# Optimization experiments

Measured on AMD Instinct MI355X. Metric: run time of the kernel, lower is better.

The kernel has to match this reference:

```python
import jax, jax.numpy as jnp
import numpy as np

SEQ, BATCH, D, N = 256, 4, 512, 32768
TEMP = 0.5


def setup_inputs() -> dict:
    key = jax.random.key(0)
    ks = jax.random.split(key, 16)
    d = D
    # xavier_uniform with gain 1/sqrt(2) for square [d,d]: limit = gain*sqrt(6/(d+d))
    lim_t = (1.0 / np.sqrt(2.0)) * np.sqrt(6.0 / (d + d))
    lim_g1 = np.sqrt(6.0 / (2 * d + d))  # default kaiming-ish scale approximated by xavier
    lim_g2 = np.sqrt(6.0 / (d + 1))
    inp = {
        "q": jax.random.normal(ks[0], (SEQ, BATCH, D), dtype=jnp.float32),
        "prev_layer_output": jax.random.normal(ks[1], (SEQ, BATCH, D), dtype=jnp.float32),
        "Wq": jax.random.uniform(ks[2], (D, D), jnp.float32, -lim_t, lim_t),
        "bq": jnp.zeros((D,), jnp.float32),
        "Wk": jax.random.uniform(ks[3], (D, D), jnp.float32, -lim_t, lim_t),
        "bk": jnp.zeros((D,), jnp.float32),
        "Wv": jax.random.uniform(ks[4], (D, D), jnp.float32, -lim_t, lim_t),
        "bv": jnp.zeros((D,), jnp.float32),
        "Wg1": jax.random.uniform(ks[5], (D, 2 * D), jnp.float32, -lim_g1, lim_g1),
        "bg1": jnp.zeros((D,), jnp.float32),
        "Wg2": jax.random.uniform(ks[6], (1, D), jnp.float32, -lim_g2, lim_g2),
        "bg2": jnp.zeros((1,), jnp.float32),
        "dstore_k": jax.random.normal(ks[7], (N, D), dtype=jnp.float32),
        "dstore_v": jax.random.normal(ks[8], (N, D), dtype=jnp.float32),
    }
    return inp


def reference(q, prev_layer_output, Wq, bq, Wk, bk, Wv, bv, Wg1, bg1, Wg2, bg2, dstore_k, dstore_v):
    # [S,B,D] -> [B,S,D]
    qb = jnp.transpose(q, (1, 0, 2))
    prevb = jnp.transpose(prev_layer_output, (1, 0, 2))
    # enable_tune projections
    _q = qb @ Wq.T + bq                      # [B,S,D]
    _k = dstore_k @ Wk.T + bk                # [N,D]
    _v = dstore_v @ Wv.T + bv                # [N,D]
    _q = _q * (D ** -0.5)
    # attention over datastore, temperature-scaled softmax
    logits = jnp.einsum("bsd,nd->bsn", _q, _k) / TEMP  # [B,S,N]
    w = jax.nn.softmax(logits, axis=-1)
    attn = jnp.einsum("bsn,nd->bsd", w, _v)            # [B,S,D]
    # gated residual fusion
    cat = jnp.concatenate([attn, prevb], axis=-1)      # [B,S,2D]
    h = jax.nn.relu(cat @ Wg1.T + bg1)                 # [B,S,D]
    sigma = jax.nn.sigmoid(h @ Wg2.T + bg2)            # [B,S,1]
    res = attn * sigma + prevb * (1.0 - sigma)
    return jnp.transpose(res, (1, 0, 2))               # [S,B,D]
```

## Files before the change

### kernel.cpp

```cpp
#include <hip/hip_runtime.h>
#include <hip/hip_bf16.h>
#include <cstdint>
#include <cstddef>


typedef unsigned short u16;
typedef u16    u16x8 __attribute__((ext_vector_type(8)));
typedef u16    u16x4 __attribute__((ext_vector_type(4)));
typedef __bf16 bf16x8 __attribute__((ext_vector_type(8)));
typedef float  f32x4 __attribute__((ext_vector_type(4)));

#define MFMA16(a, b, c) __builtin_amdgcn_mfma_f32_16x16x32_bf16( \
    __builtin_bit_cast(bf16x8, (a)), __builtin_bit_cast(bf16x8, (b)), (c), 0, 0, 0)

#define AS1 __attribute__((address_space(1)))
#define AS3 __attribute__((address_space(3)))

__device__ __forceinline__ u16 f2bf(float f) {
  unsigned u = __builtin_bit_cast(unsigned, f);
  u += 0x7fffu + ((u >> 16) & 1u);
  return (u16)(u >> 16);
}

__device__ __forceinline__ void dma16(const u16* g, u16* l) {
  __builtin_amdgcn_global_load_lds((const AS1 unsigned int*)g,
                                   (AS3 unsigned int*)l, 16, 0, 0);
}

__global__ __launch_bounds__(256) void prep_all(
    const float* __restrict__ dk, const float* __restrict__ dv,
    const float* __restrict__ Wq, const float* __restrict__ Wk,
    const float* __restrict__ bk, const float* __restrict__ bq,
    u16* __restrict__ kbf, u16* __restrict__ vt, float* __restrict__ zbase,
    float* __restrict__ cqvec, float* __restrict__ b2pre,
    float* __restrict__ cq0) {
  const int bx = blockIdx.x, t = threadIdx.x;
  if (bx < 4096) {
    __shared__ u16 Lt[64 * 72];
    const int n0 = (bx & 511) * 64, d0 = (bx >> 9) * 64;
    const int n = t >> 2, c4 = t & 3;
#pragma unroll
    for (int i = 0; i < 4; i++) {
      int col = (c4 + 4 * i) * 4;
      float4 x = *(const float4*)(dv + (size_t)(n0 + n) * 512 + d0 + col);
      Lt[(col + 0) * 72 + n] = f2bf(x.x);
      Lt[(col + 1) * 72 + n] = f2bf(x.y);
      Lt[(col + 2) * 72 + n] = f2bf(x.z);
      Lt[(col + 3) * 72 + n] = f2bf(x.w);
    }
    __syncthreads();
#pragma unroll
    for (int u = 0; u < 2; u++) {
      int unit = t + 256 * u;
      int d = unit >> 3, un = unit & 7;
      *(u16x8*)(vt + (size_t)(d0 + d) * 32768 + n0 + un * 8) =
          *(const u16x8*)&Lt[d * 72 + un * 8];
    }
  } else if (bx < 8192) {
    const int j = bx - 4096;
    size_t i0 = ((size_t)j * 256 + t) * 16;
#pragma unroll
    for (int u = 0; u < 4; u++) {
      float4 v = *(const float4*)(dk + i0 + u * 4);
      u16x4 o = {f2bf(v.x), f2bf(v.y), f2bf(v.z), f2bf(v.w)};
      *(u16x4*)(kbf + i0 + u * 4) = o;
    }
    int zi = j * 256 + t;
    if (zi < 131584) ((float4*)zbase)[zi] = make_float4(0.f, 0.f, 0.f, 0.f);
  } else if (bx < 8194) {
    int e = (bx - 8192) * 256 + t;
    float s1 = 0.f, s2 = 0.f;
    for (int d = 0; d < 512; d++) {
      s1 += bk[d] * Wq[d * 512 + e];
      s2 += bq[d] * Wk[d * 512 + e];
    }
    cqvec[e] = s1;
    b2pre[e] = s2;
  } else {
    __shared__ float red[4];
    float s = 0.f;
    for (int d = t; d < 512; d += 256) s += bq[d] * bk[d];
#pragma unroll
    for (int off = 32; off; off >>= 1) s += __shfl_down(s, off, 64);
    if ((t & 63) == 0) red[t >> 6] = s;
    __syncthreads();
    if (t == 0) cq0[0] = 0.0883883476483184f * (red[0] + red[1] + red[2] + red[3]);
  }
}

template <bool TRANSA, bool TRANSB, bool CONCAT, bool RELU, bool OUTBF16,
          bool ROWSCALE, bool CQ, bool GATE, int KK>
__global__ __launch_bounds__(256, 2) void gemm64(
    const float* __restrict__ A, const float* __restrict__ A2,
    const float* __restrict__ B, const float* __restrict__ bias,
    const float* __restrict__ lvec, const float* __restrict__ bkv,
    const float* __restrict__ wg2, float alpha, void* __restrict__ Cv,
    float* __restrict__ cqout, const float* __restrict__ cq0buf,
    float* __restrict__ sdot) {
  __shared__ u16 As[64 * 72];
  __shared__ u16 Bs[64 * 72];
  const int tid = threadIdx.x;
  const int w = tid >> 6, lane = tid & 63, quad = lane >> 4, l15 = lane & 15;
  const int m0 = blockIdx.y * 64, n0 = blockIdx.x * 64;
  const int arow = tid >> 2, ac4 = tid & 3;
  float rs = 1.0f;
  if (ROWSCALE) rs = 1.0f / lvec[m0 + arow];
  const bool docq = CQ && (blockIdx.x == 0);
  float cqacc = 0.f;
  const f32x4 fzero = {0.f, 0.f, 0.f, 0.f};
  f32x4 acc[4];
#pragma unroll
  for (int i = 0; i < 4; i++) acc[i] = fzero;

  float4 ra[4], rb[4], rk[4];
  auto loadA = [&](int k0) {
    const float* src;
    if (TRANSA)
      src = A + (size_t)(k0 + arow) * 512 + m0;
    else if (CONCAT)
      src = (k0 < 512) ? (A + (size_t)(m0 + arow) * 512 + k0)
                       : (A2 + (size_t)(m0 + arow) * 512 + (k0 - 512));
    else
      src = A + (size_t)(m0 + arow) * KK + k0;
#pragma unroll
    for (int i = 0; i < 4; i++) ra[i] = *(const float4*)(src + (ac4 + 4 * i) * 4);
  };
  auto loadB = [&](int k0) {
    const float* src = TRANSB ? (B + (size_t)(n0 + arow) * KK + k0)
                              : (B + (size_t)(k0 + arow) * 512 + n0);
#pragma unroll
    for (int i = 0; i < 4; i++) rb[i] = *(const float4*)(src + (ac4 + 4 * i) * 4);
  };
  auto loadK = [&](int k0) {
#pragma unroll
    for (int i = 0; i < 4; i++) rk[i] = *(const float4*)(bkv + k0 + (ac4 + 4 * i) * 4);
  };

  loadA(0);
  loadB(0);
  if (docq) loadK(0);
#pragma unroll
  for (int k0 = 0; k0 < KK; k0 += 64) {
    __syncthreads();
#pragma unroll
    for (int i = 0; i < 4; i++) {
      int col = (ac4 + 4 * i) * 4;
      float4 x = ra[i];
      if (ROWSCALE) { x.x *= rs; x.y *= rs; x.z *= rs; x.w *= rs; }
      if (TRANSA) {
        As[(col + 0) * 72 + arow] = f2bf(x.x);
        As[(col + 1) * 72 + arow] = f2bf(x.y);
        As[(col + 2) * 72 + arow] = f2bf(x.z);
        As[(col + 3) * 72 + arow] = f2bf(x.w);
      } else {
        u16x4 oa = {f2bf(x.x), f2bf(x.y), f2bf(x.z), f2bf(x.w)};
        *(u16x4*)&As[arow * 72 + col] = oa;
      }
      float4 y = rb[i];
      if (TRANSB) {
        u16x4 ob = {f2bf(y.x), f2bf(y.y), f2bf(y.z), f2bf(y.w)};
        *(u16x4*)&Bs[arow * 72 + col] = ob;
      } else {
        Bs[(col + 0) * 72 + arow] = f2bf(y.x);
        Bs[(col + 1) * 72 + arow] = f2bf(y.y);
        Bs[(col + 2) * 72 + arow] = f2bf(y.z);
        Bs[(col + 3) * 72 + arow] = f2bf(y.w);
      }
      if (docq)
        cqacc += ra[i].x * rk[i].x + ra[i].y * rk[i].y + ra[i].z * rk[i].z +
                 ra[i].w * rk[i].w;
    }
    if (k0 + 64 < KK) {
      loadA(k0 + 64);
      loadB(k0 + 64);
      if (docq) loadK(k0 + 64);
    }
    __syncthreads();
#pragma unroll
    for (int ks = 0; ks < 2; ks++) {
      u16x8 af = *(const u16x8*)&As[(w * 16 + l15) * 72 + ks * 32 + quad * 8];
#pragma unroll
      for (int nt = 0; nt < 4; nt++) {
        u16x8 bf = *(const u16x8*)&Bs[(nt * 16 + l15) * 72 + ks * 32 + quad * 8];
        acc[nt] = MFMA16(af, bf, acc[nt]);
      }
    }
  }

  if (docq) {
    cqacc += __shfl_xor(cqacc, 1, 64);
    cqacc += __shfl_xor(cqacc, 2, 64);
    if (ac4 == 0) cqout[m0 + arow] = alpha * cqacc + cq0buf[0];
  }
  if (GATE) {
    float part[4] = {0.f, 0.f, 0.f, 0.f};
#pragma unroll
    for (int nt = 0; nt < 4; nt++) {
      int col = n0 + nt * 16 + l15;
      float b = bias[col], wv = wg2[col];
#pragma unroll
      for (int i = 0; i < 4; i++) part[i] += fmaxf((acc[nt][i] + b) * alpha, 0.f) * wv;
    }
#pragma unroll
    for (int i = 0; i < 4; i++) {
      float v = part[i];
      v += __shfl_xor(v, 1, 64); v += __shfl_xor(v, 2, 64);
      v += __shfl_xor(v, 4, 64); v += __shfl_xor(v, 8, 64);
      if (l15 == 0) atomicAdd(&sdot[m0 + w * 16 + quad * 4 + i], v);
    }
  } else {
#pragma unroll
    for (int nt = 0; nt < 4; nt++) {
      int col = n0 + nt * 16 + l15;
      float b = bias ? bias[col] : 0.f;
#pragma unroll
      for (int i = 0; i < 4; i++) {
        int row = m0 + w * 16 + quad * 4 + i;
        float y = (acc[nt][i] + b) * alpha;
        if (RELU) y = fmaxf(y, 0.f);
        if (OUTBF16)
          ((u16*)Cv)[(size_t)row * 512 + col] = f2bf(y);
        else
          ((float*)Cv)[(size_t)row * 512 + col] = y;
      }
    }
  }
}

__global__ __launch_bounds__(512, 2) void flash(
    const u16* __restrict__ kbf,
    const u16* __restrict__ vt,
    const u16* __restrict__ q2,
    const float* __restrict__ cq,
    float* __restrict__ racc,
    float* __restrict__ lacc) {
  __shared__ u16 Ks[2][64 * 520];
  __shared__ u16 Es[2][64 * 72];
  const int tid = threadIdx.x;
  const int w = tid >> 6, lane = tid & 63, quad = lane >> 4, l15 = lane & 15;
  const int bx = blockIdx.x;
  const int xcd = bx & 7, idx = bx >> 3;
  const int qt = idx & 15, half = idx >> 4;
  const int rowbase = (xcd * 2 + half) * 2048;
  const int qbase = qt * 64;
  const int qh = w & 1, nq = w >> 1;
  const int colb = w * 64;

  u16x8 qf[2][16];
  float cqs[2];
#pragma unroll
  for (int st = 0; st < 2; st++) {
    const u16* qp = q2 + (size_t)(qbase + qh * 32 + st * 16 + l15) * 512 + quad * 8;
#pragma unroll
    for (int ks = 0; ks < 16; ks++) qf[st][ks] = *(const u16x8*)(qp + ks * 32);
    cqs[st] = cq[qbase + qh * 32 + st * 16 + l15];
  }
  const f32x4 fzero = {0.f, 0.f, 0.f, 0.f};
  f32x4 acc[4][4];
#pragma unroll
  for (int a = 0; a < 4; a++)
#pragma unroll
    for (int b = 0; b < 4; b++) acc[a][b] = fzero;
  float lp[2] = {0.f, 0.f};

  auto dma_sub = [&](int sub) {
    u16* dst = &Ks[sub & 1][(w * 8) * 520];
    const u16* g = kbf + (size_t)(rowbase + sub * 64 + w * 8) * 512 + lane * 8;
#pragma unroll
    for (int j = 0; j < 8; j++) dma16(g + (size_t)j * 512, dst + j * 520);
  };

  dma_sub(0);
  __builtin_amdgcn_s_waitcnt(0);
  __syncthreads();

#pragma unroll 1
  for (int sub = 0; sub < 32; ++sub) {
    const int buf = sub & 1;
    const int n0 = rowbase + sub * 64;
    if (sub + 1 < 32) dma_sub(sub + 1);
    u16x8 bvp[2][4];
#pragma unroll
    for (int nk = 0; nk < 2; nk++)
#pragma unroll
      for (int ct = 0; ct < 4; ct++)
        bvp[nk][ct] = *(const u16x8*)(vt + (size_t)(colb + ct * 16 + l15) * 32768 +
                                      n0 + nk * 32 + quad * 8);
    f32x4 sa[2][2];
    sa[0][0] = fzero; sa[0][1] = fzero; sa[1][0] = fzero; sa[1][1] = fzero;
#pragma unroll
    for (int ks = 0; ks < 16; ks++) {
      u16x8 af = *(const u16x8*)&Ks[buf][(nq * 16 + l15) * 520 + ks * 32 + quad * 8];
      sa[0][ks & 1] = MFMA16(af, qf[0][ks], sa[0][ks & 1]);
      sa[1][ks & 1] = MFMA16(af, qf[1][ks], sa[1][ks & 1]);
    }
#pragma unroll
    for (int st = 0; st < 2; st++) {
      f32x4 sv = sa[st][0] + sa[st][1];
      u16x4 pk;
      float ls = 0.f;
#pragma unroll
      for (int i = 0; i < 4; i++) {
        float e = __expf(sv[i] + cqs[st]);
        ls += e;
        pk[i] = f2bf(e);
      }
      lp[st] += ls;
      *(u16x4*)&Es[buf][(qh * 32 + st * 16 + l15) * 72 + nq * 16 + quad * 4] = pk;
    }
    __builtin_amdgcn_s_waitcnt(0);
    __syncthreads();
#pragma unroll
    for (int nk = 0; nk < 2; nk++) {
      u16x8 ef[4];
#pragma unroll
      for (int q2i = 0; q2i < 4; q2i++)
        ef[q2i] = *(const u16x8*)&Es[buf][(q2i * 16 + l15) * 72 + nk * 32 + quad * 8];
#pragma unroll
      for (int ct = 0; ct < 4; ct++)
#pragma unroll
        for (int q2i = 0; q2i < 4; q2i++)
          acc[q2i][ct] = MFMA16(ef[q2i], bvp[nk][ct], acc[q2i][ct]);
    }
  }
#pragma unroll
  for (int q2i = 0; q2i < 4; q2i++)
#pragma unroll
    for (int ct = 0; ct < 4; ct++) {
      int col = colb + ct * 16 + l15;
#pragma unroll
      for (int i = 0; i < 4; i++) {
        int row = qbase + q2i * 16 + quad * 4 + i;
        atomicAdd(&racc[(size_t)row * 512 + col], acc[q2i][ct][i]);
      }
    }
#pragma unroll
  for (int st = 0; st < 2; st++) {
    float v = lp[st];
    v += __shfl_xor(v, 16, 64);
    v += __shfl_xor(v, 32, 64);
    if (quad == 0) atomicAdd(&lacc[qbase + qh * 32 + st * 16 + l15], v);
  }
}

__global__ __launch_bounds__(128) void finalize(
    const float* __restrict__ sdot, const float* __restrict__ bg2,
    const float* __restrict__ attn, const float* __restrict__ prev,
    float* __restrict__ out) {
  int r = blockIdx.x, t = threadIdx.x;
  float sg = 1.f / (1.f + __expf(-(sdot[r] + bg2[0])));
  float4 a = ((const float4*)(attn + (size_t)r * 512))[t];
  float4 p = ((const float4*)(prev + (size_t)r * 512))[t];
  float4 o = {a.x * sg + p.x * (1.f - sg), a.y * sg + p.y * (1.f - sg),
              a.z * sg + p.z * (1.f - sg), a.w * sg + p.w * (1.f - sg)};
  ((float4*)(out + (size_t)r * 512))[t] = o;
}

extern "C" void kernel_launch(void* const* d_in, const int* in_sizes, int n_in,
                              void* d_out, int out_size, void* d_ws, size_t ws_size,
                              hipStream_t stream) {
  const float* q    = (const float*)d_in[0];
  const float* prev = (const float*)d_in[1];
  const float* Wq   = (const float*)d_in[2];
  const float* bq   = (const float*)d_in[3];
  const float* Wk   = (const float*)d_in[4];
  const float* bk   = (const float*)d_in[5];
  const float* Wv   = (const float*)d_in[6];
  const float* bv   = (const float*)d_in[7];
  const float* Wg1  = (const float*)d_in[8];
  const float* bg1  = (const float*)d_in[9];
  const float* Wg2  = (const float*)d_in[10];
  const float* bg2  = (const float*)d_in[11];
  const float* dk   = (const float*)d_in[12];
  const float* dv   = (const float*)d_in[13];
  float* out = (float*)d_out;

  char* ws = (char*)d_ws;
  u16*   kbf   = (u16*)(ws);
  u16*   vt    = (u16*)(ws + 33554432);
  float* racc  = (float*)(ws + 67108864);
  float* lacc  = (float*)(ws + 69206016);
  float* sdot  = (float*)(ws + 69210112);
  float* cqv   = (float*)(ws + 69214208);
  u16*   q2    = (u16*)(ws + 69218304);
  float* Wqk   = (float*)(ws + 70266880);
  float* cqvec = (float*)(ws + 71315456);
  float* b2pre = (float*)(ws + 71317504);
  float* cq0   = (float*)(ws + 71319552);
  float* attn  = (float*)(ws + 72364032);

  prep_all<<<8195, 256, 0, stream>>>(dk, dv, Wq, Wk, bk, bq, kbf, vt, racc,
                                     cqvec, b2pre, cq0);
  gemm64<true, false, false, false, false, false, false, false, 512>
      <<<dim3(8, 8), 256, 0, stream>>>(Wq, nullptr, Wk, nullptr, nullptr,
                                       nullptr, nullptr, 1.0f, Wqk, nullptr,
                                       nullptr, nullptr);
  gemm64<false, false, false, false, true, false, true, false, 512>
      <<<dim3(8, 16), 256, 0, stream>>>(q, nullptr, Wqk, b2pre, nullptr, cqvec,
                                        nullptr, 0.0883883476483184f, q2, cqv,
                                        cq0, nullptr);
  flash<<<256, 512, 0, stream>>>(kbf, vt, q2, cqv, racc, lacc);
  gemm64<false, true, false, false, false, true, false, false, 512>
      <<<dim3(8, 16), 256, 0, stream>>>(racc, nullptr, Wv, bv, lacc, nullptr,
                                        nullptr, 1.0f, attn, nullptr, nullptr,
                                        nullptr);
  gemm64<false, true, true, true, false, false, false, true, 1024>
      <<<dim3(8, 16), 256, 0, stream>>>(attn, prev, Wg1, bg1, nullptr, nullptr,
                                        Wg2, 1.0f, nullptr, nullptr, nullptr,
                                        sdot);
  finalize<<<1024, 128, 0, stream>>>(sdot, bg2, attn, prev, out);
}
```

Measured before the change: 475.8 us.

## Switch datastore attention to FP8 MFMA with chunked partials and fused prep

Converts K, V and the projected queries to FP8 (e4m3) and runs both attention matmuls with FP8 MFMA. Queries are staged in swizzled LDS, while K rows are read straight from global memory. The flash kernel now splits the datastore into 32 chunks and writes bf16 partial outputs, which a new reduce kernel sums, replacing float atomics on the output. The Wq·Wk GEMM and the bias-vector work are folded into the prep launch. The per-query bias constant is dropped because softmax normalisation cancels it. The aim is to halve the bytes moved for K/V and to use the higher FP8 MFMA throughput. The cost is much lower precision in the logits and exp weights, plus an extra partial-buffer round trip.

New measurement: 492.7 us. +3.6%, slower.

```diff
diff --git a/kernel.cpp b/kernel.cpp
--- a/kernel.cpp
+++ b/kernel.cpp
@@ -1,118 +1,62 @@
 #include <hip/hip_runtime.h>
-#include <hip/hip_bf16.h>
 #include <cstdint>
 #include <cstddef>
 
 
 typedef unsigned short u16;
-typedef u16    u16x8 __attribute__((ext_vector_type(8)));
+typedef unsigned char u8;
+typedef u8     u8x8  __attribute__((ext_vector_type(8)));
+typedef u8     u8x16 __attribute__((ext_vector_type(16)));
 typedef u16    u16x4 __attribute__((ext_vector_type(4)));
 typedef __bf16 bf16x8 __attribute__((ext_vector_type(8)));
 typedef float  f32x4 __attribute__((ext_vector_type(4)));
 
 #define MFMA16(a, b, c) __builtin_amdgcn_mfma_f32_16x16x32_bf16( \
     __builtin_bit_cast(bf16x8, (a)), __builtin_bit_cast(bf16x8, (b)), (c), 0, 0, 0)
-
-#define AS1 __attribute__((address_space(1)))
-#define AS3 __attribute__((address_space(3)))
+#define MFMA8(a, b, c) \
+    __builtin_amdgcn_mfma_f32_16x16x32_fp8_fp8((long)(a), (long)(b), (c), 0, 0, 0)
 
 __device__ __forceinline__ u16 f2bf(float f) {
   unsigned u = __builtin_bit_cast(unsigned, f);
   u += 0x7fffu + ((u >> 16) & 1u);
   return (u16)(u >> 16);
 }
-
-__device__ __forceinline__ void dma16(const u16* g, u16* l) {
-  __builtin_amdgcn_global_load_lds((const AS1 unsigned int*)g,
-                                   (AS3 unsigned int*)l, 16, 0, 0);
-}
-
-__global__ __launch_bounds__(256) void prep_all(
-    const float* __restrict__ dk, const float* __restrict__ dv,
-    const float* __restrict__ Wq, const float* __restrict__ Wk,
-    const float* __restrict__ bk, const float* __restrict__ bq,
-    u16* __restrict__ kbf, u16* __restrict__ vt, float* __restrict__ zbase,
-    float* __restrict__ cqvec, float* __restrict__ b2pre,
-    float* __restrict__ cq0) {
-  const int bx = blockIdx.x, t = threadIdx.x;
-  if (bx < 4096) {
-    __shared__ u16 Lt[64 * 72];
-    const int n0 = (bx & 511) * 64, d0 = (bx >> 9) * 64;
-    const int n = t >> 2, c4 = t & 3;
-#pragma unroll
-    for (int i = 0; i < 4; i++) {
-      int col = (c4 + 4 * i) * 4;
-      float4 x = *(const float4*)(dv + (size_t)(n0 + n) * 512 + d0 + col);
-      Lt[(col + 0) * 72 + n] = f2bf(x.x);
-      Lt[(col + 1) * 72 + n] = f2bf(x.y);
-      Lt[(col + 2) * 72 + n] = f2bf(x.z);
-      Lt[(col + 3) * 72 + n] = f2bf(x.w);
-    }
-    __syncthreads();
-#pragma unroll
-    for (int u = 0; u < 2; u++) {
-      int unit = t + 256 * u;
-      int d = unit >> 3, un = unit & 7;
-      *(u16x8*)(vt + (size_t)(d0 + d) * 32768 + n0 + un * 8) =
-          *(const u16x8*)&Lt[d * 72 + un * 8];
-    }
-  } else if (bx < 8192) {
-    const int j = bx - 4096;
-    size_t i0 = ((size_t)j * 256 + t) * 16;
-#pragma unroll
-    for (int u = 0; u < 4; u++) {
-      float4 v = *(const float4*)(dk + i0 + u * 4);
-      u16x4 o = {f2bf(v.x), f2bf(v.y), f2bf(v.z), f2bf(v.w)};
-      *(u16x4*)(kbf + i0 + u * 4) = o;
-    }
-    int zi = j * 256 + t;
-    if (zi < 131584) ((float4*)zbase)[zi] = make_float4(0.f, 0.f, 0.f, 0.f);
-  } else if (bx < 8194) {
-    int e = (bx - 8192) * 256 + t;
-    float s1 = 0.f, s2 = 0.f;
-    for (int d = 0; d < 512; d++) {
-      s1 += bk[d] * Wq[d * 512 + e];
-      s2 += bq[d] * Wk[d * 512 + e];
-    }
-    cqvec[e] = s1;
-    b2pre[e] = s2;
-  } else {
-    __shared__ float red[4];
-    float s = 0.f;
-    for (int d = t; d < 512; d += 256) s += bq[d] * bk[d];
-#pragma unroll
-    for (int off = 32; off; off >>= 1) s += __shfl_down(s, off, 64);
-    if ((t & 63) == 0) red[t >> 6] = s;
-    __syncthreads();
-    if (t == 0) cq0[0] = 0.0883883476483184f * (red[0] + red[1] + red[2] + red[3]);
-  }
-}
-
-template <bool TRANSA, bool TRANSB, bool CONCAT, bool RELU, bool OUTBF16,
-          bool ROWSCALE, bool CQ, bool GATE, int KK>
-__global__ __launch_bounds__(256, 2) void gemm64(
-    const float* __restrict__ A, const float* __restrict__ A2,
-    const float* __restrict__ B, const float* __restrict__ bias,
-    const float* __restrict__ lvec, const float* __restrict__ bkv,
-    const float* __restrict__ wg2, float alpha, void* __restrict__ Cv,
-    float* __restrict__ cqout, const float* __restrict__ cq0buf,
-    float* __restrict__ sdot) {
-  __shared__ u16 As[64 * 72];
-  __shared__ u16 Bs[64 * 72];
+__device__ __forceinline__ float bf2f(u16 h) {
+  unsigned u = ((unsigned)h) << 16;
+  return __builtin_bit_cast(float, u);
+}
+__device__ __forceinline__ u8 f2fp8(float x) {
+  return (u8)(__builtin_amdgcn_cvt_pk_fp8_f32(x, x, 0, false) & 0xff);
+}
+__device__ __forceinline__ int pk4(float4 v) {
+  int r = __builtin_amdgcn_cvt_pk_fp8_f32(v.x, v.y, 0, false);
+  return __builtin_amdgcn_cvt_pk_fp8_f32(v.z, v.w, r, true);
+}
+
+typedef u16 u16x8 __attribute__((ext_vector_type(8)));
+
+template <bool TRANSA, bool TRANSB, bool CONCAT, bool RELU, bool OUTFP8,
+          bool ROWSCALE, bool GATE, int KK>
+__device__ void gemm_core(u16* As, u16* Bs, const float* __restrict__ A,
+                          const float* __restrict__ A2,
+                          const float* __restrict__ B,
+                          const float* __restrict__ bias,
+                          const float* __restrict__ lvec,
+                          const float* __restrict__ wg2, float alpha,
+                          void* __restrict__ Cv, float* __restrict__ sdot,
+                          int bxx, int byy) {
   const int tid = threadIdx.x;
   const int w = tid >> 6, lane = tid & 63, quad = lane >> 4, l15 = lane & 15;
-  const int m0 = blockIdx.y * 64, n0 = blockIdx.x * 64;
+  const int m0 = byy * 64, n0 = bxx * 64;
   const int arow = tid >> 2, ac4 = tid & 3;
   float rs = 1.0f;
   if (ROWSCALE) rs = 1.0f / lvec[m0 + arow];
-  const bool docq = CQ && (blockIdx.x == 0);
-  float cqacc = 0.f;
   const f32x4 fzero = {0.f, 0.f, 0.f, 0.f};
   f32x4 acc[4];
 #pragma unroll
   for (int i = 0; i < 4; i++) acc[i] = fzero;
 
-  float4 ra[4], rb[4], rk[4];
+  float4 ra[4], rb[4];
   auto loadA = [&](int k0) {
     const float* src;
     if (TRANSA)
@@ -131,14 +75,9 @@
 #pragma unroll
     for (int i = 0; i < 4; i++) rb[i] = *(const float4*)(src + (ac4 + 4 * i) * 4);
   };
-  auto loadK = [&](int k0) {
-#pragma unroll
-    for (int i = 0; i < 4; i++) rk[i] = *(const float4*)(bkv + k0 + (ac4 + 4 * i) * 4);
-  };
 
   loadA(0);
   loadB(0);
-  if (docq) loadK(0);
 #pragma unroll
   for (int k0 = 0; k0 < KK; k0 += 64) {
     __syncthreads();
@@ -166,15 +105,8 @@
         Bs[(col + 2) * 72 + arow] = f2bf(y.z);
         Bs[(col + 3) * 72 + arow] = f2bf(y.w);
       }
-      if (docq)
-        cqacc += ra[i].x * rk[i].x + ra[i].y * rk[i].y + ra[i].z * rk[i].z +
-                 ra[i].w * rk[i].w;
-    }
-    if (k0 + 64 < KK) {
-      loadA(k0 + 64);
-      loadB(k0 + 64);
-      if (docq) loadK(k0 + 64);
-    }
+    }
+    if (k0 + 64 < KK) { loadA(k0 + 64); loadB(k0 + 64); }
     __syncthreads();
 #pragma unroll
     for (int ks = 0; ks < 2; ks++) {
@@ -187,11 +119,6 @@
     }
   }
 
-  if (docq) {
-    cqacc += __shfl_xor(cqacc, 1, 64);
-    cqacc += __shfl_xor(cqacc, 2, 64);
-    if (ac4 == 0) cqout[m0 + arow] = alpha * cqacc + cq0buf[0];
-  }
   if (GATE) {
     float part[4] = {0.f, 0.f, 0.f, 0.f};
 #pragma unroll
@@ -218,8 +145,8 @@
         int row = m0 + w * 16 + quad * 4 + i;
         float y = (acc[nt][i] + b) * alpha;
         if (RELU) y = fmaxf(y, 0.f);
-        if (OUTBF16)
-          ((u16*)Cv)[(size_t)row * 512 + col] = f2bf(y);
+        if (OUTFP8)
+          ((u8*)Cv)[(size_t)row * 512 + col] = f2fp8(y);
         else
           ((float*)Cv)[(size_t)row * 512 + col] = y;
       }
@@ -227,33 +154,104 @@
   }
 }
 
-__global__ __launch_bounds__(512, 2) void flash(
-    const u16* __restrict__ kbf,
-    const u16* __restrict__ vt,
-    const u16* __restrict__ q2,
-    const float* __restrict__ cq,
-    float* __restrict__ racc,
+template <bool TRANSA, bool TRANSB, bool CONCAT, bool RELU, bool OUTFP8,
+          bool ROWSCALE, bool GATE, int KK>
+__global__ __launch_bounds__(256, 2) void gemm64(
+    const float* __restrict__ A, const float* __restrict__ A2,
+    const float* __restrict__ B, const float* __restrict__ bias,
+    const float* __restrict__ lvec, const float* __restrict__ wg2, float alpha,
+    void* __restrict__ Cv, float* __restrict__ sdot) {
+  __shared__ u16 As[64 * 72];
+  __shared__ u16 Bs[64 * 72];
+  gemm_core<TRANSA, TRANSB, CONCAT, RELU, OUTFP8, ROWSCALE, GATE, KK>(
+      As, Bs, A, A2, B, bias, lvec, wg2, alpha, Cv, sdot, blockIdx.x,
+      blockIdx.y);
+}
+
+__global__ __launch_bounds__(256) void prep_all(
+    const float* __restrict__ dk, const float* __restrict__ dv,
+    const float* __restrict__ Wq, const float* __restrict__ Wk,
+    const float* __restrict__ bq, u8* __restrict__ kf8, u8* __restrict__ vtf8,
+    float* __restrict__ Wqk, float* __restrict__ b2pre,
+    float* __restrict__ zvec) {
+  __shared__ __align__(16) char smem[18432];
+  const int bx = blockIdx.x, t = threadIdx.x;
+  if (bx < 4096) {
+    u8* Lt = (u8*)smem;
+    const int n0 = (bx & 511) * 64, d0 = (bx >> 9) * 64;
+    const int n = t >> 2, c4 = t & 3;
+#pragma unroll
+    for (int i = 0; i < 4; i++) {
+      int col = (c4 + 4 * i) * 4;
+      float4 x = *(const float4*)(dv + (size_t)(n0 + n) * 512 + d0 + col);
+      Lt[(col + 0) * 72 + n] = f2fp8(x.x);
+      Lt[(col + 1) * 72 + n] = f2fp8(x.y);
+      Lt[(col + 2) * 72 + n] = f2fp8(x.z);
+      Lt[(col + 3) * 72 + n] = f2fp8(x.w);
+    }
+    __syncthreads();
+#pragma unroll
+    for (int u = 0; u < 2; u++) {
+      int unit = t + 256 * u;
+      int d = unit >> 3, un = unit & 7;
+      *(u8x8*)(vtf8 + (size_t)(d0 + d) * 32768 + n0 + un * 8) =
+          *(const u8x8*)&Lt[d * 72 + un * 8];
+    }
+  } else if (bx < 8192) {
+    const int j = bx - 4096;
+    size_t i0 = ((size_t)j * 256 + t) * 16;
+    const float* s = dk + i0;
+    int4 o;
+    o.x = pk4(*(const float4*)(s + 0));
+    o.y = pk4(*(const float4*)(s + 4));
+    o.z = pk4(*(const float4*)(s + 8));
+    o.w = pk4(*(const float4*)(s + 12));
+    *(int4*)(kf8 + i0) = o;
+  } else if (bx < 8256) {
+    const int id = bx - 8192;
+    gemm_core<true, false, false, false, false, false, false, 512>(
+        (u16*)smem, (u16*)(smem + 9216), Wq, nullptr, Wk, nullptr, nullptr,
+        nullptr, 1.0f, Wqk, nullptr, id & 7, id >> 3);
+  } else if (bx < 8264) {
+    float* rb = (float*)smem;
+    int c = (bx - 8256) * 64 + (t & 63), seg = t >> 6;
+    float s = 0.f;
+    for (int k = seg * 128; k < seg * 128 + 128; k++)
+      s += bq[k] * Wk[(size_t)k * 512 + c];
+    rb[t] = s;
+    __syncthreads();
+    if (t < 64) b2pre[c] = rb[t] + rb[t + 64] + rb[t + 128] + rb[t + 192];
+  } else {
+    for (int i = t; i < 2048; i += 256) zvec[i] = 0.f;
+  }
+}
+
+__global__ __launch_bounds__(512, 4) void flash(
+    const u8* __restrict__ kf8,
+    const u8* __restrict__ vtf8,
+    const u8* __restrict__ q2f8,
+    u16* __restrict__ part,
     float* __restrict__ lacc) {
-  __shared__ u16 Ks[2][64 * 520];
-  __shared__ u16 Es[2][64 * 72];
+  __shared__ u8 Qs[64 * 512];
+  __shared__ u8 Es[2][64 * 64];
   const int tid = threadIdx.x;
   const int w = tid >> 6, lane = tid & 63, quad = lane >> 4, l15 = lane & 15;
   const int bx = blockIdx.x;
-  const int xcd = bx & 7, idx = bx >> 3;
-  const int qt = idx & 15, half = idx >> 4;
-  const int rowbase = (xcd * 2 + half) * 2048;
+  const int qt = (bx >> 3) & 15;
+  const int chunk = (bx & 7) * 4 + (bx >> 7);
+  const int rowbase = chunk * 1024;
   const int qbase = qt * 64;
-  const int qh = w & 1, nq = w >> 1;
-  const int colb = w * 64;
-
-  u16x8 qf[2][16];
-  float cqs[2];
-#pragma unroll
-  for (int st = 0; st < 2; st++) {
-    const u16* qp = q2 + (size_t)(qbase + qh * 32 + st * 16 + l15) * 512 + quad * 8;
-#pragma unroll
-    for (int ks = 0; ks < 16; ks++) qf[st][ks] = *(const u16x8*)(qp + ks * 32);
-    cqs[st] = cq[qbase + qh * 32 + st * 16 + l15];
+  const int qh = w & 1, ng = w >> 1;
+
+  {
+    const int row = tid >> 3, cb = tid & 7;
+    const u8* src = q2f8 + (size_t)(qbase + row) * 512 + cb * 64;
+#pragma unroll
+    for (int i = 0; i < 4; i++) {
+      int c2 = cb * 4 + i;
+      *(u8x16*)&Qs[row * 512 + ((c2 ^ (row & 7)) << 4)] =
+          *(const u8x16*)(src + i * 16);
+    }
   }
   const f32x4 fzero = {0.f, 0.f, 0.f, 0.f};
   f32x4 acc[4][4];
@@ -261,86 +259,115 @@
   for (int a = 0; a < 4; a++)
 #pragma unroll
     for (int b = 0; b < 4; b++) acc[a][b] = fzero;
-  float lp[2] = {0.f, 0.f};
-
-  auto dma_sub = [&](int sub) {
-    u16* dst = &Ks[sub & 1][(w * 8) * 520];
-    const u16* g = kbf + (size_t)(rowbase + sub * 64 + w * 8) * 512 + lane * 8;
-#pragma unroll
-    for (int j = 0; j < 8; j++) dma16(g + (size_t)j * 512, dst + j * 520);
-  };
-
-  dma_sub(0);
-  __builtin_amdgcn_s_waitcnt(0);
+  float lp[8] = {0.f, 0.f, 0.f, 0.f, 0.f, 0.f, 0.f, 0.f};
   __syncthreads();
 
+  const int q7 = l15 & 7;
+  const int qrow0 = (qh * 32 + l15) * 512;
+  const int qh2 = quad >> 1, hb = (quad & 1) * 8;
+
 #pragma unroll 1
-  for (int sub = 0; sub < 32; ++sub) {
-    const int buf = sub & 1;
+  for (int sub = 0; sub < 16; ++sub) {
     const int n0 = rowbase + sub * 64;
-    if (sub + 1 < 32) dma_sub(sub + 1);
-    u16x8 bvp[2][4];
-#pragma unroll
-    for (int nk = 0; nk < 2; nk++)
-#pragma unroll
-      for (int ct = 0; ct < 4; ct++)
-        bvp[nk][ct] = *(const u16x8*)(vt + (size_t)(colb + ct * 16 + l15) * 32768 +
-                                      n0 + nk * 32 + quad * 8);
-    f32x4 sa[2][2];
-    sa[0][0] = fzero; sa[0][1] = fzero; sa[1][0] = fzero; sa[1][1] = fzero;
+    long kf[16];
+    const u8* kp = kf8 + (size_t)(n0 + ng * 16 + l15) * 512 + quad * 8;
+#pragma unroll
+    for (int ks = 0; ks < 16; ks++) kf[ks] = *(const long*)(kp + ks * 32);
+    f32x4 sa0 = fzero, sa1 = fzero;
 #pragma unroll
     for (int ks = 0; ks < 16; ks++) {
-      u16x8 af = *(const u16x8*)&Ks[buf][(nq * 16 + l15) * 520 + ks * 32 + quad * 8];
-      sa[0][ks & 1] = MFMA16(af, qf[0][ks], sa[0][ks & 1]);
-      sa[1][ks & 1] = MFMA16(af, qf[1][ks], sa[1][ks & 1]);
-    }
-#pragma unroll
-    for (int st = 0; st < 2; st++) {
-      f32x4 sv = sa[st][0] + sa[st][1];
-      u16x4 pk;
-      float ls = 0.f;
+      int cidx = (((ks * 2 + qh2) ^ q7) << 4) + hb;
+      long a0 = *(const long*)&Qs[qrow0 + cidx];
+      long a1 = *(const long*)&Qs[qrow0 + 16 * 512 + cidx];
+      sa0 = MFMA8(a0, kf[ks], sa0);
+      sa1 = MFMA8(a1, kf[ks], sa1);
+    }
+    u8* ew = Es[sub & 1];
+    const int n = ng * 16 + l15;
+#pragma unroll
+    for (int qa = 0; qa < 2; qa++) {
+      f32x4 sv = qa ? sa1 : sa0;
+      float e0 = __expf(sv[0] * 0.0625f);
+      float e1 = __expf(sv[1] * 0.0625f);
+      float e2 = __expf(sv[2] * 0.0625f);
+      float e3 = __expf(sv[3] * 0.0625f);
+      lp[qa * 4 + 0] += e0; lp[qa * 4 + 1] += e1;
+      lp[qa * 4 + 2] += e2; lp[qa * 4 + 3] += e3;
+      int pk = __builtin_amdgcn_cvt_pk_fp8_f32(e0, e1, 0, false);
+      pk = __builtin_amdgcn_cvt_pk_fp8_f32(e2, e3, pk, true);
 #pragma unroll
       for (int i = 0; i < 4; i++) {
-        float e = __expf(sv[i] + cqs[st]);
-        ls += e;
-        pk[i] = f2bf(e);
-      }
-      lp[st] += ls;
-      *(u16x4*)&Es[buf][(qh * 32 + st * 16 + l15) * 72 + nq * 16 + quad * 4] = pk;
-    }
-    __builtin_amdgcn_s_waitcnt(0);
+        int q = qh * 32 + qa * 16 + quad * 4 + i;
+        ew[q * 64 + ((((n >> 3) ^ (q & 7))) << 3) + (n & 7)] =
+            (u8)(pk >> (8 * i));
+      }
+    }
+    long vf[4][2];
+#pragma unroll
+    for (int dt = 0; dt < 4; dt++)
+#pragma unroll
+      for (int nk = 0; nk < 2; nk++)
+        vf[dt][nk] = *(const long*)(vtf8 +
+                                    (size_t)(w * 64 + dt * 16 + l15) * 32768 +
+                                    n0 + nk * 32 + quad * 8);
     __syncthreads();
+    const u8* er = Es[sub & 1];
 #pragma unroll
     for (int nk = 0; nk < 2; nk++) {
-      u16x8 ef[4];
-#pragma unroll
-      for (int q2i = 0; q2i < 4; q2i++)
-        ef[q2i] = *(const u16x8*)&Es[buf][(q2i * 16 + l15) * 72 + nk * 32 + quad * 8];
-#pragma unroll
-      for (int ct = 0; ct < 4; ct++)
-#pragma unroll
-        for (int q2i = 0; q2i < 4; q2i++)
-          acc[q2i][ct] = MFMA16(ef[q2i], bvp[nk][ct], acc[q2i][ct]);
-    }
-  }
-#pragma unroll
-  for (int q2i = 0; q2i < 4; q2i++)
-#pragma unroll
-    for (int ct = 0; ct < 4; ct++) {
-      int col = colb + ct * 16 + l15;
-#pragma unroll
-      for (int i = 0; i < 4; i++) {
-        int row = qbase + q2i * 16 + quad * 4 + i;
-        atomicAdd(&racc[(size_t)row * 512 + col], acc[q2i][ct][i]);
-      }
-    }
-#pragma unroll
-  for (int st = 0; st < 2; st++) {
-    float v = lp[st];
-    v += __shfl_xor(v, 16, 64);
-    v += __shfl_xor(v, 32, 64);
-    if (quad == 0) atomicAdd(&lacc[qbase + qh * 32 + st * 16 + l15], v);
-  }
+      long ef[4];
+#pragma unroll
+      for (int qt4 = 0; qt4 < 4; qt4++) {
+        int q = qt4 * 16 + l15;
+        ef[qt4] = *(const long*)&er[q * 64 + ((((nk * 4 + quad) ^ (q & 7))) << 3)];
+      }
+#pragma unroll
+      for (int dt = 0; dt < 4; dt++)
+#pragma unroll
+        for (int qt4 = 0; qt4 < 4; qt4++)
+          acc[dt][qt4] = MFMA8(vf[dt][nk], ef[qt4], acc[dt][qt4]);
+    }
+  }
+#pragma unroll
+  for (int qt4 = 0; qt4 < 4; qt4++) {
+    int qq = qbase + qt4 * 16 + l15;
+#pragma unroll
+    for (int dt = 0; dt < 4; dt++) {
+      u16x4 o = {f2bf(acc[dt][qt4][0]), f2bf(acc[dt][qt4][1]),
+                 f2bf(acc[dt][qt4][2]), f2bf(acc[dt][qt4][3])};
+      *(u16x4*)(part + ((size_t)qq * 32 + chunk) * 512 + w * 64 + dt * 16 +
+                quad * 4) = o;
+    }
+  }
+#pragma unroll
+  for (int j = 0; j < 8; j++) {
+    float v = lp[j];
+    v += __shfl_xor(v, 1, 64); v += __shfl_xor(v, 2, 64);
+    v += __shfl_xor(v, 4, 64); v += __shfl_xor(v, 8, 64);
+    lp[j] = v;
+  }
+  if (l15 == 0) {
+#pragma unroll
+    for (int qa = 0; qa < 2; qa++)
+#pragma unroll
+      for (int i = 0; i < 4; i++)
+        atomicAdd(&lacc[qbase + qh * 32 + qa * 16 + quad * 4 + i],
+                  lp[qa * 4 + i]);
+  }
+}
+
+__global__ __launch_bounds__(256) void reduce_racc(const u16* __restrict__ part,
+                                                   float* __restrict__ racc) {
+  const int q = blockIdx.x, t = threadIdx.x;
+  const u16* p = part + (size_t)q * 32 * 512 + t * 2;
+  float s0 = 0.f, s1 = 0.f;
+#pragma unroll
+  for (int c = 0; c < 32; c++) {
+    unsigned v = *(const unsigned*)(p + c * 512);
+    s0 += bf2f((u16)(v & 0xffff));
+    s1 += bf2f((u16)(v >> 16));
+  }
+  float2 o = {s0, s1};
+  *(float2*)(racc + (size_t)q * 512 + t * 2) = o;
 }
 
 __global__ __launch_bounds__(128) void finalize(
@@ -364,7 +391,6 @@
   const float* Wq   = (const float*)d_in[2];
   const float* bq   = (const float*)d_in[3];
   const float* Wk   = (const float*)d_in[4];
-  const float* bk   = (const float*)d_in[5];
   const float* Wv   = (const float*)d_in[6];
   const float* bv   = (const float*)d_in[7];
   const float* Wg1  = (const float*)d_in[8];
@@ -376,37 +402,30 @@
   float* out = (float*)d_out;
 
   char* ws = (char*)d_ws;
-  u16*   kbf   = (u16*)(ws);
-  u16*   vt    = (u16*)(ws + 33554432);
+  u8*    kf8   = (u8*)(ws);
+  u8*    vtf8  = (u8*)(ws + 16777216);
+  u16*   part  = (u16*)(ws + 33554432);
   float* racc  = (float*)(ws + 67108864);
   float* lacc  = (float*)(ws + 69206016);
   float* sdot  = (float*)(ws + 69210112);
-  float* cqv   = (float*)(ws + 69214208);
-  u16*   q2    = (u16*)(ws + 69218304);
-  float* Wqk   = (float*)(ws + 70266880);
-  float* cqvec = (float*)(ws + 71315456);
-  float* b2pre = (float*)(ws + 71317504);
-  float* cq0   = (float*)(ws + 71319552);
-  float* attn  = (float*)(ws + 72364032);
-
-  prep_all<<<8195, 256, 0, stream>>>(dk, dv, Wq, Wk, bk, bq, kbf, vt, racc,
-                                     cqvec, b2pre, cq0);
-  gemm64<true, false, false, false, false, false, false, false, 512>
-      <<<dim3(8, 8), 256, 0, stream>>>(Wq, nullptr, Wk, nullptr, nullptr,
-                                       nullptr, nullptr, 1.0f, Wqk, nullptr,
-                                       nullptr, nullptr);
-  gemm64<false, false, false, false, true, false, true, false, 512>
-      <<<dim3(8, 16), 256, 0, stream>>>(q, nullptr, Wqk, b2pre, nullptr, cqvec,
-                                        nullptr, 0.0883883476483184f, q2, cqv,
-                                        cq0, nullptr);
-  flash<<<256, 512, 0, stream>>>(kbf, vt, q2, cqv, racc, lacc);
-  gemm64<false, true, false, false, false, true, false, false, 512>
+  u8*    q2f8  = (u8*)(ws + 69214208);
+  float* Wqk   = (float*)(ws + 69738496);
+  float* b2pre = (float*)(ws + 70787072);
+  float* attn  = (float*)(ws + 70791168);
+
+  prep_all<<<8265, 256, 0, stream>>>(dk, dv, Wq, Wk, bq, kf8, vtf8, Wqk, b2pre,
+                                     lacc);
+  gemm64<false, false, false, false, true, false, false, 512>
+      <<<dim3(8, 16), 256, 0, stream>>>(q, nullptr, Wqk, b2pre, nullptr,
+                                        nullptr, 1.4142135623730951f, q2f8,
+                                        nullptr);
+  flash<<<512, 512, 0, stream>>>(kf8, vtf8, q2f8, part, lacc);
+  reduce_racc<<<1024, 256, 0, stream>>>(part, racc);
+  gemm64<false, true, false, false, false, true, false, 512>
       <<<dim3(8, 16), 256, 0, stream>>>(racc, nullptr, Wv, bv, lacc, nullptr,
-                                        nullptr, 1.0f, attn, nullptr, nullptr,
-                                        nullptr);
-  gemm64<false, true, true, true, false, false, false, true, 1024>
-      <<<dim3(8, 16), 256, 0, stream>>>(attn, prev, Wg1, bg1, nullptr, nullptr,
-                                        Wg2, 1.0f, nullptr, nullptr, nullptr,
-                                        sdot);
+                                        1.0f, attn, nullptr);
+  gemm64<false, true, true, true, false, false, true, 1024>
+      <<<dim3(8, 16), 256, 0, stream>>>(attn, prev, Wg1, bg1, nullptr, Wg2,
+                                        1.0f, nullptr, sdot);
   finalize<<<1024, 128, 0, stream>>>(sdot, bg2, attn, prev, out);
 }
```
